# Optimization experiments

Measured on AMD Instinct MI355X. Metric: run time of the kernel, lower is better.

## Reference

```python
import jax, jax.numpy as jnp
import numpy as np


def setup_inputs() -> dict:
    key = jax.random.key(0)
    k1, k2, k3, k4 = jax.random.split(key, 4)
    B, T, D, HS = 4, 2048, 1024, 64
    x = jax.random.normal(k1, (B, T, D), dtype=jnp.float32)
    # nn.Linear(d_model, head_size, bias=False) weights: (head_size, d_model)
    s = 1.0 / np.sqrt(D)
    Wk = jax.random.normal(k2, (HS, D), dtype=jnp.float32) * s
    Wq = jax.random.normal(k3, (HS, D), dtype=jnp.float32) * s
    Wv = jax.random.normal(k4, (HS, D), dtype=jnp.float32) * s
    return {"x": x, "Wk": Wk, "Wq": Wq, "Wv": Wv}


def reference(x, Wk, Wq, Wv):
    # x: [B, T, D]; W*: [HS, D]
    B, T, D = x.shape
    HS = Wk.shape[0]
    k = jnp.einsum('btd,hd->bth', x, Wk)  # [B, T, HS]
    q = jnp.einsum('btd,hd->bth', x, Wq)
    v = jnp.einsum('btd,hd->bth', x, Wv)
    # FAITHFUL to source bug: scores / hs**(-0.5) == scores * sqrt(hs)
    scale = jnp.asarray(np.sqrt(HS), dtype=x.dtype)
    scores = jnp.einsum('bqh,bkh->bqk', q, k) * scale  # [B, T, T]
    causal = jnp.tril(jnp.ones((T, T), dtype=bool))
    scores = jnp.where(causal, scores, jnp.asarray(-jnp.inf, dtype=scores.dtype))
    att = jax.nn.softmax(scores, axis=-1)  # dropout p=0.0 -> identity
    out = jnp.einsum('bqk,bkh->bqh', att, v)  # [B, T, HS]
    return out
```

## Files before the change

kernel.cpp:

```cpp
#include <hip/hip_runtime.h>

#define TSEQ 2048
#define DDIM 1024
#define HSZ  64
#define NB   4
#define NROWS (NB * TSEQ)

typedef short bf16x8 __attribute__((ext_vector_type(8)));
typedef short s16x4  __attribute__((ext_vector_type(4)));
typedef float f32x4  __attribute__((ext_vector_type(4)));
typedef unsigned int u32;

#define MFMA16(a, b, c) __builtin_amdgcn_mfma_f32_16x16x32_bf16((a), (b), (c), 0, 0, 0)

__device__ inline void split_rn(float f, short& hi, short& lo) {
    u32 u = __builtin_bit_cast(u32, f);
    u32 rr = (u + 0x7fffu + ((u >> 16) & 1u)) & 0xffff0000u;
    hi = (short)(rr >> 16);
    float fh = __builtin_bit_cast(float, rr);
    float fl = f - fh;
    lo = (short)(__builtin_bit_cast(u32, fl) >> 16);
}
__device__ inline short bf16rn(float f) {
    u32 u = __builtin_bit_cast(u32, f);
    return (short)((u + 0x7fffu + ((u >> 16) & 1u)) >> 16);
}

__global__ __launch_bounds__(256) void wsplit_kernel(
    const float* __restrict__ Wk, const float* __restrict__ Wq, const float* __restrict__ Wv,
    short* __restrict__ wbhi, short* __restrict__ wblo)
{
    int i = blockIdx.x * 256 + threadIdx.x;
    int off = i << 2;
    int which = off >> 16;
    int loc = off & 65535;
    const float* src = (which == 0) ? Wk : (which == 1) ? Wq : Wv;
    float4 v = *(const float4*)(src + loc);
    short h0,h1,h2,h3, l0,l1,l2,l3;
    split_rn(v.x, h0, l0); split_rn(v.y, h1, l1);
    split_rn(v.z, h2, l2); split_rn(v.w, h3, l3);
    *(s16x4*)(wbhi + off) = (s16x4){h0,h1,h2,h3};
    *(s16x4*)(wblo + off) = (s16x4){l0,l1,l2,l3};
}

__global__ __launch_bounds__(256, 3) void proj_mfma(
    const float* __restrict__ x,
    const short* __restrict__ wbhi, const short* __restrict__ wblo,
    short* __restrict__ khi, short* __restrict__ klo,
    short* __restrict__ qhi, short* __restrict__ qlo,
    short* __restrict__ vthi)
{
    __shared__ __align__(16) short xh[64][88], xl[64][88];
    __shared__ __align__(16) short wh[64][88], wl[64][88];

    const int tid  = threadIdx.x;
    const int wv   = tid >> 6;
    const int lane = tid & 63;
    const int g    = lane >> 4;
    const int c    = lane & 15;
    const int mode = blockIdx.y;
    const long rb  = (long)blockIdx.x * 64;

    const int srow = tid >> 2;
    const int skq  = (tid & 3) << 4;
    const float* xp  = x + (rb + srow) * DDIM + skq;
    const short* whp = wbhi + mode * (HSZ * DDIM) + srow * DDIM + skq;
    const short* wlp = wblo + mode * (HSZ * DDIM) + srow * DDIM + skq;

    f32x4 acc[4];
    acc[0] = 0; acc[1] = 0; acc[2] = 0; acc[3] = 0;

    for (int k0 = 0; k0 < DDIM; k0 += 64) {
        {
            float4 f0 = *(const float4*)(xp + k0);
            float4 f1 = *(const float4*)(xp + k0 + 4);
            float4 f2 = *(const float4*)(xp + k0 + 8);
            float4 f3 = *(const float4*)(xp + k0 + 12);
            float fv[16] = {f0.x,f0.y,f0.z,f0.w, f1.x,f1.y,f1.z,f1.w,
                            f2.x,f2.y,f2.z,f2.w, f3.x,f3.y,f3.z,f3.w};
            short hh[16], ll[16];
            #pragma unroll
            for (int j = 0; j < 16; ++j) split_rn(fv[j], hh[j], ll[j]);
            #pragma unroll
            for (int u = 0; u < 2; ++u) {
                *(bf16x8*)&xh[srow][skq + 8*u] = *(bf16x8*)&hh[8*u];
                *(bf16x8*)&xl[srow][skq + 8*u] = *(bf16x8*)&ll[8*u];
            }
        }
        {
            bf16x8 a0 = *(const bf16x8*)(whp + k0);
            bf16x8 a1 = *(const bf16x8*)(whp + k0 + 8);
            bf16x8 b0 = *(const bf16x8*)(wlp + k0);
            bf16x8 b1 = *(const bf16x8*)(wlp + k0 + 8);
            *(bf16x8*)&wh[srow][skq]     = a0;
            *(bf16x8*)&wh[srow][skq + 8] = a1;
            *(bf16x8*)&wl[srow][skq]     = b0;
            *(bf16x8*)&wl[srow][skq + 8] = b1;
        }
        __syncthreads();

        #pragma unroll
        for (int kk = 0; kk < 2; ++kk) {
            bf16x8 ah = *(const bf16x8*)&xh[16*wv + c][kk*32 + 8*g];
            bf16x8 al = *(const bf16x8*)&xl[16*wv + c][kk*32 + 8*g];
            __builtin_amdgcn_s_setprio(1);
            #pragma unroll
            for (int ct = 0; ct < 4; ++ct) {
                bf16x8 bh = *(const bf16x8*)&wh[ct*16 + c][kk*32 + 8*g];
                bf16x8 bl = *(const bf16x8*)&wl[ct*16 + c][kk*32 + 8*g];
                acc[ct] = MFMA16(al, bh, acc[ct]);
                acc[ct] = MFMA16(ah, bl, acc[ct]);
                acc[ct] = MFMA16(ah, bh, acc[ct]);
            }
            __builtin_amdgcn_s_setprio(0);
        }
        __syncthreads();
    }

    const int batch = (int)(rb >> 11);
    const int t0    = (int)(rb & 2047);
    if (mode < 2) {
        short* oh = mode ? qhi : khi;
        short* ol = mode ? qlo : klo;
        const float sc = mode ? 8.0f : 1.0f;
        #pragma unroll
        for (int ct = 0; ct < 4; ++ct) {
            #pragma unroll
            for (int r = 0; r < 4; ++r) {
                long row = rb + 16*wv + 4*g + r;
                short h, lo2; split_rn(acc[ct][r] * sc, h, lo2);
                oh[row * HSZ + ct*16 + c] = h;
                ol[row * HSZ + ct*16 + c] = lo2;
            }
        }
    } else {
        #pragma unroll
        for (int ct = 0; ct < 4; ++ct)
            #pragma unroll
            for (int r = 0; r < 4; ++r)
                wh[ct*16 + c][16*wv + 4*g + r] = bf16rn(acc[ct][r]);
        __syncthreads();
        const int d = tid >> 2, t16 = (tid & 3) << 4;
        long gofs = ((long)(batch * HSZ + d)) * TSEQ + t0 + t16;
        *(bf16x8*)(vthi + gofs)     = *(const bf16x8*)&wh[d][t16];
        *(bf16x8*)(vthi + gofs + 8) = *(const bf16x8*)&wh[d][t16 + 8];
    }
}

__global__ __launch_bounds__(512, 4) void attn_mfma(
    const short* __restrict__ qhi, const short* __restrict__ qlo,
    const short* __restrict__ khi, const short* __restrict__ klo,
    const short* __restrict__ vthi,
    float* __restrict__ out)
{
    __shared__ __align__(16) short pbuf[8][16][88];
    __shared__ float obuf[4][16][68];
    __shared__ float mlbuf[8][16][2];

    const int tid  = threadIdx.x;
    const int w    = tid >> 6;
    const int lane = tid & 63;
    const int g    = lane >> 4;
    const int c    = lane & 15;

    const int bid   = blockIdx.x;
    const int work  = ((bid & 7) << 6) | (bid >> 3);
    const int batch = work >> 7;
    const int rank  = work & 127;
    const int tile  = (rank < 64) ? (127 - 2*rank) : (126 - 2*(rank - 64));
    const int qb0   = tile << 4;
    const long bb   = (long)batch * TSEQ;
    const int lastkey = qb0 + 15;

    bf16x8 qh[2], ql[2];
    {
        const long qofs = (bb + qb0 + c) * HSZ;
        #pragma unroll
        for (int kk = 0; kk < 2; ++kk) {
            qh[kk] = *(const bf16x8*)(qhi + qofs + kk*32 + 8*g);
            ql[kk] = *(const bf16x8*)(qlo + qofs + kk*32 + 8*g);
        }
    }

    f32x4 oacc[4];
    #pragma unroll
    for (int dt = 0; dt < 4; ++dt) oacc[dt] = 0;
    float m = -1e30f, l = 0.0f;

    if (64 * w <= lastkey) {
        const int nsteps = ((lastkey - 64 * w) >> 9) + 1;
        for (int s = 0; s < nsteps; ++s) {
            const int jb = (s << 9) + (w << 6);
            f32x4 sa[4];
            sa[0] = 0; sa[1] = 0; sa[2] = 0; sa[3] = 0;
            #pragma unroll
            for (int kk = 0; kk < 2; ++kk) {
                bf16x8 kb_h[4], kb_l[4];
                #pragma unroll
                for (int t = 0; t < 4; ++t) {
                    const long kofs = (bb + jb + t*16 + c) * HSZ + kk*32 + 8*g;
                    kb_h[t] = *(const bf16x8*)(khi + kofs);
                    kb_l[t] = *(const bf16x8*)(klo + kofs);
                }
                __builtin_amdgcn_s_setprio(1);
                #pragma unroll
                for (int t = 0; t < 4; ++t) {
                    sa[t] = MFMA16(kb_h[t], ql[kk], sa[t]);
                    sa[t] = MFMA16(kb_l[t], qh[kk], sa[t]);
                    sa[t] = MFMA16(kb_h[t], qh[kk], sa[t]);
                }
                __builtin_amdgcn_s_setprio(0);
            }
            bf16x8 vb[2][4];
            #pragma unroll
            for (int kk = 0; kk < 2; ++kk)
                #pragma unroll
                for (int dt = 0; dt < 4; ++dt) {
                    const long vofs = ((long)(batch * HSZ + dt*16 + c)) * TSEQ + jb + kk*32 + 8*g;
                    vb[kk][dt] = *(const bf16x8*)(vthi + vofs);
                }
            if (jb + 63 > qb0) {
                #pragma unroll
                for (int t = 0; t < 4; ++t) {
                    const int kb0 = jb + t*16 + 4*g;
                    #pragma unroll
                    for (int r = 0; r < 4; ++r)
                        if (kb0 + r > qb0 + c) sa[t][r] = -1e30f;
                }
            }
            float mx = sa[0][0];
            #pragma unroll
            for (int t = 0; t < 4; ++t)
                #pragma unroll
                for (int r = 0; r < 4; ++r) mx = fmaxf(mx, sa[t][r]);
            mx = fmaxf(mx, __shfl_xor(mx, 16));
            mx = fmaxf(mx, __shfl_xor(mx, 32));
            const float mold = m;
            const float mn = fmaxf(mold, mx);
            float rs = 0.0f;
            #pragma unroll
            for (int t = 0; t < 4; ++t) {
                float p0 = __expf(sa[t][0] - mn);
                float p1 = __expf(sa[t][1] - mn);
                float p2 = __expf(sa[t][2] - mn);
                float p3 = __expf(sa[t][3] - mn);
                rs += (p0 + p1) + (p2 + p3);
                u32 w0 = (u32)(unsigned short)bf16rn(p0) | ((u32)(unsigned short)bf16rn(p1) << 16);
                u32 w1 = (u32)(unsigned short)bf16rn(p2) | ((u32)(unsigned short)bf16rn(p3) << 16);
                *(u32*)&pbuf[w][c][t*16 + 4*g]     = w0;
                *(u32*)&pbuf[w][c][t*16 + 4*g + 2] = w1;
            }
            rs += __shfl_xor(rs, 16);
            rs += __shfl_xor(rs, 32);
            const float fs = __expf(mold - mn);
            l = l * fs + rs;
            m = mn;
            if (__any(mn > mold)) {
                float fr[4];
                #pragma unroll
                for (int r = 0; r < 4; ++r) fr[r] = __shfl(fs, 16*g + 4*g + r);
                #pragma unroll
                for (int dt = 0; dt < 4; ++dt) {
                    oacc[dt][0] *= fr[0]; oacc[dt][1] *= fr[1];
                    oacc[dt][2] *= fr[2]; oacc[dt][3] *= fr[3];
                }
            }
            #pragma unroll
            for (int kk = 0; kk < 2; ++kk) {
                bf16x8 pa = *(const bf16x8*)&pbuf[w][c][kk*32 + 8*g];
                __builtin_amdgcn_s_setprio(1);
                #pragma unroll
                for (int dt = 0; dt < 4; ++dt)
                    oacc[dt] = MFMA16(pa, vb[kk][dt], oacc[dt]);
                __builtin_amdgcn_s_setprio(0);
            }
        }
    }

    if (lane < 16) { mlbuf[w][lane][0] = m; mlbuf[w][lane][1] = l; }
    __syncthreads();
    float fw_[4], linv_[4];
    #pragma unroll
    for (int r = 0; r < 4; ++r) {
        const int row = 4*g + r;
        float ms = mlbuf[0][row][0];
        #pragma unroll
        for (int wv = 1; wv < 8; ++wv) ms = fmaxf(ms, mlbuf[wv][row][0]);
        float ls = 0.0f;
        #pragma unroll
        for (int wv = 0; wv < 8; ++wv)
            ls += __expf(mlbuf[wv][row][0] - ms) * mlbuf[wv][row][1];
        fw_[r] = __expf(mlbuf[w][row][0] - ms);
        linv_[r] = 1.0f / ls;
    }
    #pragma unroll
    for (int dt = 0; dt < 4; ++dt) {
        oacc[dt][0] *= fw_[0]; oacc[dt][1] *= fw_[1];
        oacc[dt][2] *= fw_[2]; oacc[dt][3] *= fw_[3];
    }
    if (w >= 4)
        #pragma unroll
        for (int dt = 0; dt < 4; ++dt)
            #pragma unroll
            for (int r = 0; r < 4; ++r)
                obuf[w-4][4*g + r][dt*16 + c] = oacc[dt][r];
    __syncthreads();
    if (w < 4)
        #pragma unroll
        for (int dt = 0; dt < 4; ++dt)
            #pragma unroll
            for (int r = 0; r < 4; ++r)
                oacc[dt][r] += obuf[w][4*g + r][dt*16 + c];
    if (w == 2 || w == 3)
        #pragma unroll
        for (int dt = 0; dt < 4; ++dt)
            #pragma unroll
            for (int r = 0; r < 4; ++r)
                obuf[w][4*g + r][dt*16 + c] = oacc[dt][r];
    __syncthreads();
    if (w == 0)
        #pragma unroll
        for (int dt = 0; dt < 4; ++dt)
            #pragma unroll
            for (int r = 0; r < 4; ++r)
                oacc[dt][r] += obuf[2][4*g + r][dt*16 + c];
    if (w == 1) {
        #pragma unroll
        for (int dt = 0; dt < 4; ++dt)
            #pragma unroll
            for (int r = 0; r < 4; ++r) {
                oacc[dt][r] += obuf[3][4*g + r][dt*16 + c];
                obuf[1][4*g + r][dt*16 + c] = oacc[dt][r];
            }
    }
    __syncthreads();
    if (w == 0) {
        #pragma unroll
        for (int dt = 0; dt < 4; ++dt)
            #pragma unroll
            for (int r = 0; r < 4; ++r) {
                float val = (oacc[dt][r] + obuf[1][4*g + r][dt*16 + c]) * linv_[r];
                out[(bb + qb0 + 4*g + r) * HSZ + dt*16 + c] = val;
            }
    }
}

extern "C" void kernel_launch(void* const* d_in, const int* in_sizes, int n_in,
                              void* d_out, int out_size, void* d_ws, size_t ws_size,
                              hipStream_t stream) {
    const float* x  = (const float*)d_in[0];
    const float* Wk = (const float*)d_in[1];
    const float* Wq = (const float*)d_in[2];
    const float* Wv = (const float*)d_in[3];
    float* out = (float*)d_out;

    short* ws = (short*)d_ws;
    const size_t SEG = (size_t)NROWS * HSZ;
    short* khi  = ws;
    short* klo  = ws + SEG;
    short* qhi  = ws + 2*SEG;
    short* qlo  = ws + 3*SEG;
    short* vthi = ws + 4*SEG;
    short* wbhi = ws + 5*SEG;
    short* wblo = wbhi + 3*HSZ*DDIM;

    wsplit_kernel<<<192, 256, 0, stream>>>(Wk, Wq, Wv, wbhi, wblo);
    proj_mfma<<<dim3(128, 3), 256, 0, stream>>>(x, wbhi, wblo,
                                                khi, klo, qhi, qlo, vthi);
    attn_mfma<<<512, 512, 0, stream>>>(qhi, qlo, khi, klo, vthi, out);
}
```

Baseline: 135.6 us.

## Prefetch next projection tile into registers and defer V loads in attention

The projection GEMM loop now issues the global loads for the next K-slice of x and the split weights right after the barrier, so they overlap the current MFMA work instead of being loaded at the top of each iteration. In the attention kernel, V loads move from before the softmax to inside the PV loop, one kk slice at a time, which lowers live register pressure at the cost of exposing load latency closer to use. The pbuf and obuf shared arrays now alias one buffer to reduce LDS footprint, which needs extra barriers in the reduction epilogue. The lane index expression for the rescale shuffle is simplified to an equivalent form.

```diff
diff --git a/kernel.cpp b/kernel.cpp
--- a/kernel.cpp
+++ b/kernel.cpp
@@ -70,34 +70,44 @@
     f32x4 acc[4];
     acc[0] = 0; acc[1] = 0; acc[2] = 0; acc[3] = 0;
 
+    float4 f0 = *(const float4*)(xp);
+    float4 f1 = *(const float4*)(xp + 4);
+    float4 f2 = *(const float4*)(xp + 8);
+    float4 f3 = *(const float4*)(xp + 12);
+    bf16x8 a0 = *(const bf16x8*)(whp);
+    bf16x8 a1 = *(const bf16x8*)(whp + 8);
+    bf16x8 b0 = *(const bf16x8*)(wlp);
+    bf16x8 b1 = *(const bf16x8*)(wlp + 8);
+
     for (int k0 = 0; k0 < DDIM; k0 += 64) {
         {
-            float4 f0 = *(const float4*)(xp + k0);
-            float4 f1 = *(const float4*)(xp + k0 + 4);
-            float4 f2 = *(const float4*)(xp + k0 + 8);
-            float4 f3 = *(const float4*)(xp + k0 + 12);
             float fv[16] = {f0.x,f0.y,f0.z,f0.w, f1.x,f1.y,f1.z,f1.w,
                             f2.x,f2.y,f2.z,f2.w, f3.x,f3.y,f3.z,f3.w};
             short hh[16], ll[16];
             #pragma unroll
             for (int j = 0; j < 16; ++j) split_rn(fv[j], hh[j], ll[j]);
-            #pragma unroll
-            for (int u = 0; u < 2; ++u) {
-                *(bf16x8*)&xh[srow][skq + 8*u] = *(bf16x8*)&hh[8*u];
-                *(bf16x8*)&xl[srow][skq + 8*u] = *(bf16x8*)&ll[8*u];
-            }
-        }
-        {
-            bf16x8 a0 = *(const bf16x8*)(whp + k0);
-            bf16x8 a1 = *(const bf16x8*)(whp + k0 + 8);
-            bf16x8 b0 = *(const bf16x8*)(wlp + k0);
-            bf16x8 b1 = *(const bf16x8*)(wlp + k0 + 8);
+            *(bf16x8*)&xh[srow][skq]     = *(bf16x8*)&hh[0];
+            *(bf16x8*)&xh[srow][skq + 8] = *(bf16x8*)&hh[8];
+            *(bf16x8*)&xl[srow][skq]     = *(bf16x8*)&ll[0];
+            *(bf16x8*)&xl[srow][skq + 8] = *(bf16x8*)&ll[8];
             *(bf16x8*)&wh[srow][skq]     = a0;
             *(bf16x8*)&wh[srow][skq + 8] = a1;
             *(bf16x8*)&wl[srow][skq]     = b0;
             *(bf16x8*)&wl[srow][skq + 8] = b1;
         }
         __syncthreads();
+
+        if (k0 + 64 < DDIM) {
+            const int kn = k0 + 64;
+            f0 = *(const float4*)(xp + kn);
+            f1 = *(const float4*)(xp + kn + 4);
+            f2 = *(const float4*)(xp + kn + 8);
+            f3 = *(const float4*)(xp + kn + 12);
+            a0 = *(const bf16x8*)(whp + kn);
+            a1 = *(const bf16x8*)(whp + kn + 8);
+            b0 = *(const bf16x8*)(wlp + kn);
+            b1 = *(const bf16x8*)(wlp + kn + 8);
+        }
 
         #pragma unroll
         for (int kk = 0; kk < 2; ++kk) {
@@ -153,8 +163,9 @@
     const short* __restrict__ vthi,
     float* __restrict__ out)
 {
-    __shared__ __align__(16) short pbuf[8][16][88];
-    __shared__ float obuf[4][16][68];
+    __shared__ __align__(16) char smem[22528];
+    short (*pbuf)[16][88] = (short(*)[16][88])smem;
+    float (*obuf)[16][68] = (float(*)[16][68])smem;
     __shared__ float mlbuf[8][16][2];
 
     const int tid  = threadIdx.x;
@@ -211,14 +222,6 @@
                 }
                 __builtin_amdgcn_s_setprio(0);
             }
-            bf16x8 vb[2][4];
-            #pragma unroll
-            for (int kk = 0; kk < 2; ++kk)
-                #pragma unroll
-                for (int dt = 0; dt < 4; ++dt) {
-                    const long vofs = ((long)(batch * HSZ + dt*16 + c)) * TSEQ + jb + kk*32 + 8*g;
-                    vb[kk][dt] = *(const bf16x8*)(vthi + vofs);
-                }
             if (jb + 63 > qb0) {
                 #pragma unroll
                 for (int t = 0; t < 4; ++t) {
@@ -258,7 +261,7 @@
             if (__any(mn > mold)) {
                 float fr[4];
                 #pragma unroll
-                for (int r = 0; r < 4; ++r) fr[r] = __shfl(fs, 16*g + 4*g + r);
+                for (int r = 0; r < 4; ++r) fr[r] = __shfl(fs, 20*g + r);
                 #pragma unroll
                 for (int dt = 0; dt < 4; ++dt) {
                     oacc[dt][0] *= fr[0]; oacc[dt][1] *= fr[1];
@@ -268,10 +271,16 @@
             #pragma unroll
             for (int kk = 0; kk < 2; ++kk) {
                 bf16x8 pa = *(const bf16x8*)&pbuf[w][c][kk*32 + 8*g];
+                bf16x8 vb[4];
+                #pragma unroll
+                for (int dt = 0; dt < 4; ++dt) {
+                    const long vofs = ((long)(batch * HSZ + dt*16 + c)) * TSEQ + jb + kk*32 + 8*g;
+                    vb[dt] = *(const bf16x8*)(vthi + vofs);
+                }
                 __builtin_amdgcn_s_setprio(1);
                 #pragma unroll
                 for (int dt = 0; dt < 4; ++dt)
-                    oacc[dt] = MFMA16(pa, vb[kk][dt], oacc[dt]);
+                    oacc[dt] = MFMA16(pa, vb[dt], oacc[dt]);
                 __builtin_amdgcn_s_setprio(0);
             }
         }
@@ -298,6 +307,7 @@
         oacc[dt][0] *= fw_[0]; oacc[dt][1] *= fw_[1];
         oacc[dt][2] *= fw_[2]; oacc[dt][3] *= fw_[3];
     }
+    __syncthreads();
     if (w >= 4)
         #pragma unroll
         for (int dt = 0; dt < 4; ++dt)
@@ -311,6 +321,7 @@
             #pragma unroll
             for (int r = 0; r < 4; ++r)
                 oacc[dt][r] += obuf[w][4*g + r][dt*16 + c];
+    __syncthreads();
     if (w == 2 || w == 3)
         #pragma unroll
         for (int dt = 0; dt < 4; ++dt)
```

Result: faster. 132.2 us (-2.5%).
